# Performance work log

Measured on AMD Instinct MI355X. Metric: run time of the kernel, lower is better.

The kernel has to match this reference:

```python
import jax, jax.numpy as jnp
import numpy as np

B, S, D, H = 4, 4096, 1024, 8
HD = D // H  # head dims, FFT length for circular convolution


def setup_inputs() -> dict:
    key = jax.random.key(0)
    k1, k2, k3 = jax.random.split(key, 3)
    x = jax.random.normal(k1, (B, S, D), dtype=jnp.float32)
    # torch nn.Linear(D, 3D, bias=False) -> store as [D, 3D] for x @ W
    w_qkv = jax.random.normal(k2, (D, 3 * D), dtype=jnp.float32) * (1.0 / np.sqrt(D))
    w_out = jax.random.normal(k3, (D, D), dtype=jnp.float32) * (1.0 / np.sqrt(D))
    return {"x": x, "w_qkv": w_qkv, "w_out": w_out}


def reference(x, w_qkv, w_out):
    # HRR self-attention (causal, norm=False, dropout in eval mode => identity).
    b, s, d = x.shape
    qkv = x @ w_qkv                               # [B,S,3D]
    q, k, v = jnp.split(qkv, 3, axis=-1)
    q = q.reshape(b, s, H, HD)
    k = k.reshape(b, s, H, HD)
    v = v.reshape(b, s, H, HD)
    # Holographic binding: circular convolution k (*) v == ifft(fft(k)*fft(v))
    fq = jnp.fft.fft(q, axis=-1)                  # [B,S,H,HD] complex
    fk = jnp.fft.fft(k, axis=-1)
    fv = jnp.fft.fft(v, axis=-1)
    kv = fk * fv                                  # bound key-value pairs (freq domain)
    kv = jnp.cumsum(kv, axis=1)                   # causal aggregation over sequence
    # Unbinding via circular correlation with the query: ifft(S * conj(fft(q)))
    vals = jnp.fft.ifft(kv * jnp.conj(fq), axis=-1).real.astype(x.dtype)
    vals = vals.reshape(b, s, d)
    return vals @ w_out
```

## Files before the change

### kernel.cpp

```cpp
#include <hip/hip_runtime.h>

static constexpr int BB = 4;
static constexpr int SS = 4096;
static constexpr int DD = 1024;
static constexpr int HH = 8;
static constexpr int HD = 128;
static constexpr int CS = 32;
static constexpr int NCHUNK = SS / CS;
static constexpr int MROWS = BB * SS;

typedef __attribute__((ext_vector_type(8))) short bfrag;
typedef __attribute__((ext_vector_type(4))) float floatx4;

__device__ __forceinline__ float bf2f(unsigned int u) {
    return __uint_as_float((u & 0xFFFFu) << 16);
}
__device__ __forceinline__ unsigned short f2bf(float f) {
    unsigned int x = __float_as_uint(f);
    unsigned int r = x + 0x7FFFu + ((x >> 16) & 1u);
    return (unsigned short)(r >> 16);
}
__device__ __forceinline__ unsigned int pack_rne(float a, float b) {
    return ((unsigned int)f2bf(a)) | (((unsigned int)f2bf(b)) << 16);
}

__device__ __forceinline__ void async_copy16(const void* g, void* l) {
    __builtin_amdgcn_global_load_lds(
        (const __attribute__((address_space(1))) unsigned int*)g,
        (__attribute__((address_space(3))) unsigned int*)l, 16, 0, 0);
}

struct cpx { float re, im; };

__device__ __forceinline__ cpx cadd(cpx a, cpx b) { return {a.re + b.re, a.im + b.im}; }
__device__ __forceinline__ cpx csub(cpx a, cpx b) { return {a.re - b.re, a.im - b.im}; }
__device__ __forceinline__ cpx cmul(cpx a, cpx b) {
    return { fmaf(a.re, b.re, -a.im * b.im), fmaf(a.re, b.im, a.im * b.re) };
}
__device__ __forceinline__ cpx cmul_cj(cpx a, cpx b) {
    return { fmaf(a.re, b.re, a.im * b.im), fmaf(a.im, b.re, -a.re * b.im) };
}
__device__ __forceinline__ cpx shflx(cpx x, int m) {
    return { __shfl_xor(x.re, m), __shfl_xor(x.im, m) };
}
__device__ __forceinline__ cpx shfl_at(cpx x, int src) {
    return { __shfl(x.re, src), __shfl(x.im, src) };
}

__device__ __forceinline__ int pair_lane_even(int l) {
    int m = (int)(__brev((unsigned)l) >> 26);
    int mp = (64 - m) & 63;
    return (int)(__brev((unsigned)mp) >> 26);
}

__device__ __forceinline__ void make_tw(int lane, cpx tw[7]) {
    const float NEG2PI = -6.28318530717958647692f;
    float a0 = NEG2PI * (float)lane * (1.0f / 128.0f);
    tw[0] = { __cosf(a0), __sinf(a0) };
    int d = 32;
#pragma unroll
    for (int s = 1; s <= 6; ++s) {
        int i = lane & (d - 1);
        float a = NEG2PI * (float)i / (float)(2 * d);
        tw[s] = { __cosf(a), __sinf(a) };
        d >>= 1;
    }
}

__device__ __forceinline__ void fft128_fwd(cpx& x0, cpx& x1, const cpx tw[7], int lane) {
    cpx a = x0, b = x1;
    x0 = cadd(a, b);
    x1 = cmul(csub(a, b), tw[0]);
    int d = 32;
#pragma unroll
    for (int s = 1; s <= 6; ++s) {
        const bool up = (lane & d) != 0;
        cpx o0 = shflx(x0, d);
        cpx o1 = shflx(x1, d);
        cpx s0 = cadd(x0, o0);
        cpx s1 = cadd(x1, o1);
        cpx d0 = cmul(csub(o0, x0), tw[s]);
        cpx d1 = cmul(csub(o1, x1), tw[s]);
        x0 = up ? d0 : s0;
        x1 = up ? d1 : s1;
        d >>= 1;
    }
}

__device__ __forceinline__ void fft128_inv(cpx& x0, cpx& x1, const cpx tw[7], int lane) {
    int d = 1;
#pragma unroll
    for (int s = 6; s >= 1; --s) {
        const bool up = (lane & d) != 0;
        cpx o0 = shflx(x0, d);
        cpx o1 = shflx(x1, d);
        cpx b0 = up ? x0 : o0;
        cpx a0 = up ? o0 : x0;
        cpx b1 = up ? x1 : o1;
        cpx a1 = up ? o1 : x1;
        cpx t0 = cmul_cj(b0, tw[s]);
        cpx t1 = cmul_cj(b1, tw[s]);
        x0 = up ? csub(a0, t0) : cadd(a0, t0);
        x1 = up ? csub(a1, t1) : cadd(a1, t1);
        d <<= 1;
    }
    cpx t = cmul_cj(x1, tw[0]);
    cpx a = x0;
    const float inv = 0.0078125f;
    x0 = { (a.re + t.re) * inv, (a.im + t.im) * inv };
    x1 = { (a.re - t.re) * inv, (a.im - t.im) * inv };
}

__global__ __launch_bounds__(256) void convert_bf16(const float* __restrict__ X,
                                                    unsigned short* __restrict__ Y)
{
    const size_t i = ((size_t)blockIdx.x * 256 + threadIdx.x) * 8;
    float4 v0 = *reinterpret_cast<const float4*>(X + i);
    float4 v1 = *reinterpret_cast<const float4*>(X + i + 4);
    uint4 p = { pack_rne(v0.x, v0.y), pack_rne(v0.z, v0.w),
                pack_rne(v1.x, v1.y), pack_rne(v1.z, v1.w) };
    *reinterpret_cast<uint4*>(Y + i) = p;
}

__global__ __launch_bounds__(256) void transpose_rn(const float* __restrict__ W,
                                                    unsigned short* __restrict__ T,
                                                    int K, int N)
{
    __shared__ float tile[32][33];
    const int n0 = blockIdx.x * 32, k0 = blockIdx.y * 32;
    const int r = threadIdx.x >> 5, c = threadIdx.x & 31;
#pragma unroll
    for (int i = 0; i < 4; ++i)
        tile[r + 8 * i][c] = W[(size_t)(k0 + r + 8 * i) * N + n0 + c];
    __syncthreads();
#pragma unroll
    for (int i = 0; i < 4; ++i) {
        float v = tile[c][r + 8 * i];
        T[(size_t)(n0 + r + 8 * i) * K + k0 + c] = f2bf(v);
    }
}

template <typename OutT>
__global__ __launch_bounds__(512, 2) void gemm256(const unsigned short* __restrict__ A,
                                                  const unsigned short* __restrict__ Bt,
                                                  OutT* __restrict__ C,
                                                  int M, int N, int K)
{
    extern __shared__ __align__(16) unsigned short lds[];

    const int tid = threadIdx.x, lane = tid & 63, w = tid >> 6;
    const int wr = w >> 2, wc = w & 3;

    const int nbx = N >> 8;
    const int cpx_ = gridDim.x >> 3;
    const int wg = blockIdx.x;
    const int swz = (wg & 7) * cpx_ + (wg >> 3);
    const int n0 = (swz % nbx) << 8;
    const int m0 = (swz / nbx) << 8;

    const int lr = lane >> 2;
    const int kx = (((lane & 3) ^ ((lane >> 3) & 3)) << 3);
    const unsigned short* gA = A  + (size_t)(m0 + 32 * w + lr) * K + kx;
    const unsigned short* gB = Bt + (size_t)(n0 + 32 * w + lr) * K + kx;

    auto stageA = [&](int buf, int kk, int kelem) {
        unsigned short* dst = lds + buf * 32768 + kk * 8192 + (32 * w) * 32;
        const unsigned short* src = gA + kelem;
        async_copy16(src, dst);
        async_copy16(src + (size_t)16 * K, dst + 512);
    };
    auto stageB = [&](int buf, int kk, int kelem) {
        unsigned short* dst = lds + buf * 32768 + 16384 + kk * 8192 + (32 * w) * 32;
        const unsigned short* src = gB + kelem;
        async_copy16(src, dst);
        async_copy16(src + (size_t)16 * K, dst + 512);
    };

    const int sl = lane >> 4;
    const int xa = ((lane & 15) >> 1) & 3;
    const int soff = ((sl ^ xa) << 3);
    const int ra = (wr * 128 + (lane & 15)) * 32 + soff;
    const int rb = (wc * 64  + (lane & 15)) * 32 + soff;

    floatx4 acc[8][4];
#pragma unroll
    for (int m = 0; m < 8; ++m)
#pragma unroll
        for (int n = 0; n < 4; ++n) { floatx4 z = {0.f, 0.f, 0.f, 0.f}; acc[m][n] = z; }

    const int NT = K >> 6;

    stageA(0, 0, 0);  stageB(0, 0, 0);
    stageA(0, 1, 32); stageB(0, 1, 32);
    if (NT > 1) { stageA(1, 0, 64); stageB(1, 0, 64); }
    asm volatile("s_waitcnt vmcnt(8)" ::: "memory");
    __builtin_amdgcn_s_barrier();

    for (int i = 0; i < NT; ++i) {
        const int bb = (i & 1) * 32768;
        bfrag af0[4], af1[4], bf0[4], bf1[4];

        {
            const unsigned short* pA = lds + bb + ra;
            const unsigned short* pB = lds + bb + 16384 + rb;
#pragma unroll
            for (int m = 0; m < 4; ++m) af0[m] = *reinterpret_cast<const bfrag*>(pA + m * 512);
#pragma unroll
            for (int n = 0; n < 4; ++n) bf0[n] = *reinterpret_cast<const bfrag*>(pB + n * 512);
            if (i + 1 < NT) stageB((i + 1) & 1, 1, (i + 1) * 64 + 32);
            __builtin_amdgcn_s_barrier();
            __builtin_amdgcn_s_setprio(1);
#pragma unroll
            for (int m = 0; m < 4; ++m)
#pragma unroll
                for (int n = 0; n < 4; ++n)
                    acc[m][n] = __builtin_amdgcn_mfma_f32_16x16x32_bf16(af0[m], bf0[n], acc[m][n], 0, 0, 0);
            __builtin_amdgcn_s_setprio(0);
            __builtin_amdgcn_s_barrier();
        }

        {
            const unsigned short* pA = lds + bb + ra + 2048;
#pragma unroll
            for (int m = 0; m < 4; ++m) af1[m] = *reinterpret_cast<const bfrag*>(pA + m * 512);
            if (i + 1 < NT) {
                stageA((i + 1) & 1, 1, (i + 1) * 64 + 32);
                asm volatile("s_waitcnt vmcnt(6)" ::: "memory");
            } else {
                asm volatile("s_waitcnt vmcnt(0)" ::: "memory");
            }
            __builtin_amdgcn_s_barrier();
            __builtin_amdgcn_s_setprio(1);
#pragma unroll
            for (int m = 0; m < 4; ++m)
#pragma unroll
                for (int n = 0; n < 4; ++n)
                    acc[4 + m][n] = __builtin_amdgcn_mfma_f32_16x16x32_bf16(af1[m], bf0[n], acc[4 + m][n], 0, 0, 0);
            __builtin_amdgcn_s_setprio(0);
            __builtin_amdgcn_s_barrier();
        }

        {
            const unsigned short* pA = lds + bb + 8192 + ra;
            const unsigned short* pB = lds + bb + 16384 + 8192 + rb;
#pragma unroll
            for (int m = 0; m < 4; ++m) af0[m] = *reinterpret_cast<const bfrag*>(pA + m * 512);
#pragma unroll
            for (int n = 0; n < 4; ++n) bf1[n] = *reinterpret_cast<const bfrag*>(pB + n * 512);
            if (i + 2 < NT) stageB(i & 1, 0, (i + 2) * 64);
            __builtin_amdgcn_s_barrier();
            __builtin_amdgcn_s_setprio(1);
#pragma unroll
            for (int m = 0; m < 4; ++m)
#pragma unroll
                for (int n = 0; n < 4; ++n)
                    acc[m][n] = __builtin_amdgcn_mfma_f32_16x16x32_bf16(af0[m], bf1[n], acc[m][n], 0, 0, 0);
            __builtin_amdgcn_s_setprio(0);
            __builtin_amdgcn_s_barrier();
        }

        {
            const unsigned short* pA = lds + bb + 8192 + ra + 2048;
#pragma unroll
            for (int m = 0; m < 4; ++m) af1[m] = *reinterpret_cast<const bfrag*>(pA + m * 512);
            if (i + 2 < NT) {
                stageA(i & 1, 0, (i + 2) * 64);
                asm volatile("s_waitcnt vmcnt(6)" ::: "memory");
            } else if (i + 1 < NT) {
                asm volatile("s_waitcnt vmcnt(2)" ::: "memory");
            } else {
                asm volatile("s_waitcnt vmcnt(0)" ::: "memory");
            }
            __builtin_amdgcn_s_barrier();
            __builtin_amdgcn_s_setprio(1);
#pragma unroll
            for (int m = 0; m < 4; ++m)
#pragma unroll
                for (int n = 0; n < 4; ++n)
                    acc[4 + m][n] = __builtin_amdgcn_mfma_f32_16x16x32_bf16(af1[m], bf1[n], acc[4 + m][n], 0, 0, 0);
            __builtin_amdgcn_s_setprio(0);
            __builtin_amdgcn_s_barrier();
        }
    }

    if constexpr (sizeof(OutT) == 2) {
        unsigned short* myt = lds + w * 8192;
#pragma unroll
        for (int m = 0; m < 8; ++m)
#pragma unroll
            for (int n = 0; n < 4; ++n)
#pragma unroll
                for (int r = 0; r < 4; ++r)
                    myt[(m * 16 + sl * 4 + r) * 64 + n * 16 + (lane & 15)] = f2bf(acc[m][n][r]);
        asm volatile("s_waitcnt lgkmcnt(0)" ::: "memory");
#pragma unroll
        for (int c = 0; c < 16; ++c) {
            const int idx = c * 64 + lane;
            const int row = idx >> 3, cc = (idx & 7) << 3;
            uint4 v = *reinterpret_cast<const uint4*>(myt + idx * 8);
            *reinterpret_cast<uint4*>(C + (size_t)(m0 + wr * 128 + row) * N + (n0 + wc * 64 + cc)) = v;
        }
    } else {
        float* myf = reinterpret_cast<float*>(lds) + w * 4096;
#pragma unroll
        for (int pass = 0; pass < 2; ++pass) {
#pragma unroll
            for (int mp = 0; mp < 4; ++mp) {
                const int m = pass * 4 + mp;
#pragma unroll
                for (int n = 0; n < 4; ++n)
#pragma unroll
                    for (int r = 0; r < 4; ++r)
                        myf[(mp * 16 + sl * 4 + r) * 64 + n * 16 + (lane & 15)] = acc[m][n][r];
            }
            asm volatile("s_waitcnt lgkmcnt(0)" ::: "memory");
#pragma unroll
            for (int c = 0; c < 16; ++c) {
                const int idx = c * 64 + lane;
                const int row = idx >> 4;
                const int cc = (idx & 15) << 2;
                float4 v = *reinterpret_cast<const float4*>(myf + row * 64 + cc);
                *reinterpret_cast<float4*>(
                    C + (size_t)(m0 + wr * 128 + pass * 64 + row) * N + (n0 + wc * 64 + cc)) = v;
            }
            asm volatile("s_waitcnt lgkmcnt(0)" ::: "memory");
        }
    }
}

__global__ __launch_bounds__(256) void hrr_phaseA(const unsigned short* __restrict__ qkv,
                                                  unsigned int* __restrict__ P,
                                                  float* __restrict__ totals)
{
    const int blk = blockIdx.x;
    const int bh = blk / NCHUNK;
    const int chunk = blk % NCHUNK;
    const int b = bh >> 3, h = bh & 7;
    const int tid = threadIdx.x;
    const int wave = tid >> 6, lane = tid & 63;

    cpx tw[7];
    make_tw(lane, tw);
    const int pl0 = pair_lane_even(lane);
    const int pl1 = lane ^ 63;

    cpx acc0 = {0.f, 0.f}, acc1 = {0.f, 0.f};
    const int s0 = chunk * CS + wave * (CS / 4);
    for (int i = 0; i < CS / 4; ++i) {
        const int s = s0 + i;
        const unsigned short* base = qkv + (size_t)(b * SS + s) * 3072 + h * 128;
        cpx z0 = { bf2f(base[1024 + lane]),      bf2f(base[2048 + lane]) };
        cpx z1 = { bf2f(base[1024 + 64 + lane]), bf2f(base[2048 + 64 + lane]) };
        fft128_fwd(z0, z1, tw, lane);
        cpx sq0 = cmul(z0, z0);
        cpx sq1 = cmul(z1, z1);
        cpx sp0 = shfl_at(sq0, pl0);
        cpx sp1 = shfl_at(sq1, pl1);
        cpx p0 = { 0.25f * (sq0.im + sp0.im), 0.25f * (sp0.re - sq0.re) };
        cpx p1 = { 0.25f * (sq1.im + sp1.im), 0.25f * (sp1.re - sq1.re) };
        acc0 = cadd(acc0, p0);
        acc1 = cadd(acc1, p1);
        unsigned int* prow = P + ((size_t)bh * SS + s) * 128;
        prow[lane]      = pack_rne(p0.re, p0.im);
        prow[64 + lane] = pack_rne(p1.re, p1.im);
    }

    __shared__ float red[4][256];
    red[wave][lane * 2 + 0] = acc0.re;
    red[wave][lane * 2 + 1] = acc0.im;
    red[wave][128 + lane * 2 + 0] = acc1.re;
    red[wave][128 + lane * 2 + 1] = acc1.im;
    __syncthreads();

    float s4 = red[0][tid] + red[1][tid] + red[2][tid] + red[3][tid];
    totals[((size_t)bh * NCHUNK + chunk) * 256 + tid] = s4;
}

__global__ __launch_bounds__(256) void hrr_phaseB(float* __restrict__ totals)
{
    const int bh = blockIdx.x;
    const int t = threadIdx.x;
    float run = 0.f;
#pragma unroll 4
    for (int c = 0; c < NCHUNK; ++c) {
        const size_t idx = ((size_t)bh * NCHUNK + c) * 256 + t;
        float v = totals[idx];
        totals[idx] = run;
        run += v;
    }
}

__global__ __launch_bounds__(256) void hrr_phaseC(const unsigned short* __restrict__ qkv,
                                                  const unsigned int* __restrict__ P,
                                                  const float* __restrict__ totals,
                                                  unsigned short* __restrict__ vals)
{
    __shared__ float Pf[CS * 256];

    const int blk = blockIdx.x;
    const int bh = blk / NCHUNK;
    const int chunk = blk % NCHUNK;
    const int b = bh >> 3, h = bh & 7;
    const int tid = threadIdx.x;
    const int wave = tid >> 6, lane = tid & 63;

    cpx tw[7];
    make_tw(lane, tw);
    const int pl0 = pair_lane_even(lane);
    const int pl1 = lane ^ 63;

#pragma unroll
    for (int it = 0; it < CS / 4; ++it) {
        const int sl = it * 4 + wave;
        const int s = chunk * CS + sl;
        const unsigned int* prow = P + ((size_t)bh * SS + s) * 128;
        unsigned int a = prow[lane];
        unsigned int c = prow[64 + lane];
        float2 fa = { bf2f(a), bf2f(a >> 16) };
        float2 fc = { bf2f(c), bf2f(c >> 16) };
        *reinterpret_cast<float2*>(&Pf[sl * 256 + 2 * lane]) = fa;
        *reinterpret_cast<float2*>(&Pf[sl * 256 + 128 + 2 * lane]) = fc;
    }
    __syncthreads();

    {
        float run = totals[((size_t)bh * NCHUNK + chunk) * 256 + tid];
#pragma unroll 8
        for (int s = 0; s < CS; ++s) {
            run += Pf[s * 256 + tid];
            Pf[s * 256 + tid] = run;
        }
    }
    __syncthreads();

    for (int i = 0; i < CS / 8; ++i) {
        const int sl = wave * (CS / 4) + 2 * i;
        const int s1 = chunk * CS + sl;
        const unsigned short* b1 = qkv + (size_t)(b * SS + s1) * 3072 + h * 128;
        const unsigned short* b2 = b1 + 3072;
        cpx z0 = { bf2f(b1[lane]),      bf2f(b2[lane]) };
        cpx z1 = { bf2f(b1[64 + lane]), bf2f(b2[64 + lane]) };
        fft128_fwd(z0, z1, tw, lane);
        cpx B0 = shfl_at(z0, pl0);
        cpx B1 = shfl_at(z1, pl1);
        cpx cf1_0 = { 0.5f * (z0.re + B0.re), 0.5f * (B0.im - z0.im) };
        cpx cf1_1 = { 0.5f * (z1.re + B1.re), 0.5f * (B1.im - z1.im) };
        cpx cf2_0 = { 0.5f * (z0.im + B0.im), 0.5f * (z0.re - B0.re) };
        cpx cf2_1 = { 0.5f * (z1.im + B1.im), 0.5f * (z1.re - B1.re) };

        const float* r1 = &Pf[sl * 256];
        const float* r2 = r1 + 256;
        float2 t0 = *reinterpret_cast<const float2*>(&r1[2 * lane]);
        float2 t1 = *reinterpret_cast<const float2*>(&r1[128 + 2 * lane]);
        float2 t2 = *reinterpret_cast<const float2*>(&r2[2 * lane]);
        float2 t3 = *reinterpret_cast<const float2*>(&r2[128 + 2 * lane]);
        cpx C1_0 = { t0.x, t0.y }, C1_1 = { t1.x, t1.y };
        cpx C2_0 = { t2.x, t2.y }, C2_1 = { t3.x, t3.y };

        cpx a0 = cmul(C1_0, cf1_0), w0 = cmul(C2_0, cf2_0);
        cpx a1 = cmul(C1_1, cf1_1), w1 = cmul(C2_1, cf2_1);
        cpx u0 = { a0.re - w0.im, a0.im + w0.re };
        cpx u1 = { a1.re - w1.im, a1.im + w1.re };
        fft128_inv(u0, u1, tw, lane);

        unsigned short* o1 = vals + (size_t)(b * SS + s1) * DD + h * 128;
        unsigned short* o2 = o1 + DD;
        o1[lane]      = f2bf(u0.re);
        o1[64 + lane] = f2bf(u1.re);
        o2[lane]      = f2bf(u0.im);
        o2[64 + lane] = f2bf(u1.im);
    }
}

extern "C" void kernel_launch(void* const* d_in, const int* in_sizes, int n_in,
                              void* d_out, int out_size, void* d_ws, size_t ws_size,
                              hipStream_t stream) {
    const float* x     = (const float*)d_in[0];
    const float* w_qkv = (const float*)d_in[1];
    const float* w_out = (const float*)d_in[2];
    float* out = (float*)d_out;

    unsigned short* qkv  = (unsigned short*)d_ws;
    unsigned short* xb   = qkv + (size_t)MROWS * 3072;
    unsigned short* vals = xb + (size_t)MROWS * DD;
    unsigned int* P      = (unsigned int*)(vals + (size_t)MROWS * DD);
    float* totals        = (float*)(P + (size_t)32 * SS * 128);
    unsigned short* wqkvt = (unsigned short*)(totals + (size_t)32 * NCHUNK * 256);
    unsigned short* woutt = wqkvt + (size_t)3072 * 1024;

    static bool attr_done = false;
    if (!attr_done) {
        hipFuncSetAttribute(reinterpret_cast<const void*>(gemm256<unsigned short>),
                            hipFuncAttributeMaxDynamicSharedMemorySize, 131072);
        hipFuncSetAttribute(reinterpret_cast<const void*>(gemm256<float>),
                            hipFuncAttributeMaxDynamicSharedMemorySize, 131072);
        attr_done = true;
    }

    convert_bf16<<<(MROWS * DD) / (256 * 8), 256, 0, stream>>>(x, xb);
    transpose_rn<<<dim3(3072 / 32, 1024 / 32), 256, 0, stream>>>(w_qkv, wqkvt, 1024, 3072);
    transpose_rn<<<dim3(1024 / 32, 1024 / 32), 256, 0, stream>>>(w_out, woutt, 1024, 1024);

    gemm256<unsigned short><<<(3072 / 256) * (MROWS / 256), 512, 131072, stream>>>(
        xb, wqkvt, qkv, MROWS, 3072, DD);

    hrr_phaseA<<<BB * HH * NCHUNK, 256, 0, stream>>>(qkv, P, totals);

    hrr_phaseB<<<BB * HH, 256, 0, stream>>>(totals);

    hrr_phaseC<<<BB * HH * NCHUNK, 256, 0, stream>>>(qkv, P, totals, vals);

    gemm256<float><<<(DD / 256) * (MROWS / 256), 512, 131072, stream>>>(
        vals, woutt, out, MROWS, DD, DD);
}
```

Measured before the change: 369.0 us.

## Stage HRR scan inputs and outputs through LDS with async 16-byte copies

```diff
diff --git a/kernel.cpp b/kernel.cpp
--- a/kernel.cpp
+++ b/kernel.cpp
@@ -332,6 +332,9 @@
                                                   unsigned int* __restrict__ P,
                                                   float* __restrict__ totals)
 {
+    __shared__ __align__(16) unsigned short Sk[CS * 128];
+    __shared__ __align__(16) unsigned short Sv[CS * 128];
+
     const int blk = blockIdx.x;
     const int bh = blk / NCHUNK;
     const int chunk = blk % NCHUNK;
@@ -339,18 +342,33 @@
     const int tid = threadIdx.x;
     const int wave = tid >> 6, lane = tid & 63;
 
+    {
+        const size_t rowbase = (size_t)(b * SS + chunk * CS) * 3072 + h * 128;
+#pragma unroll
+        for (int q = 0; q < 2; ++q) {
+            const int r = 8 * wave + 4 * q + (lane >> 4);
+            const unsigned short* srcK = qkv + rowbase + (size_t)r * 3072 + 1024 + (lane & 15) * 8;
+            const unsigned short* srcV = srcK + 1024;
+            async_copy16(srcK, Sk + (8 * wave + 4 * q) * 128);
+            async_copy16(srcV, Sv + (8 * wave + 4 * q) * 128);
+        }
+    }
+
     cpx tw[7];
     make_tw(lane, tw);
     const int pl0 = pair_lane_even(lane);
     const int pl1 = lane ^ 63;
 
+    __syncthreads();
+
     cpx acc0 = {0.f, 0.f}, acc1 = {0.f, 0.f};
     const int s0 = chunk * CS + wave * (CS / 4);
     for (int i = 0; i < CS / 4; ++i) {
-        const int s = s0 + i;
-        const unsigned short* base = qkv + (size_t)(b * SS + s) * 3072 + h * 128;
-        cpx z0 = { bf2f(base[1024 + lane]),      bf2f(base[2048 + lane]) };
-        cpx z1 = { bf2f(base[1024 + 64 + lane]), bf2f(base[2048 + 64 + lane]) };
+        const int sl = wave * (CS / 4) + i;
+        const unsigned short* kk = Sk + sl * 128;
+        const unsigned short* vv = Sv + sl * 128;
+        cpx z0 = { bf2f(kk[lane]),      bf2f(vv[lane]) };
+        cpx z1 = { bf2f(kk[64 + lane]), bf2f(vv[64 + lane]) };
         fft128_fwd(z0, z1, tw, lane);
         cpx sq0 = cmul(z0, z0);
         cpx sq1 = cmul(z1, z1);
@@ -360,7 +378,7 @@
         cpx p1 = { 0.25f * (sq1.im + sp1.im), 0.25f * (sp1.re - sq1.re) };
         acc0 = cadd(acc0, p0);
         acc1 = cadd(acc1, p1);
-        unsigned int* prow = P + ((size_t)bh * SS + s) * 128;
+        unsigned int* prow = P + ((size_t)bh * SS + s0 + i) * 128;
         prow[lane]      = pack_rne(p0.re, p0.im);
         prow[64 + lane] = pack_rne(p1.re, p1.im);
     }
@@ -376,10 +394,10 @@
     totals[((size_t)bh * NCHUNK + chunk) * 256 + tid] = s4;
 }
 
-__global__ __launch_bounds__(256) void hrr_phaseB(float* __restrict__ totals)
+__global__ __launch_bounds__(64) void hrr_phaseB(float* __restrict__ totals)
 {
-    const int bh = blockIdx.x;
-    const int t = threadIdx.x;
+    const int bh = blockIdx.x >> 2;
+    const int t = (blockIdx.x & 3) * 64 + threadIdx.x;
     float run = 0.f;
 #pragma unroll 4
     for (int c = 0; c < NCHUNK; ++c) {
@@ -396,6 +414,8 @@
                                                   unsigned short* __restrict__ vals)
 {
     __shared__ float Pf[CS * 256];
+    __shared__ __align__(16) unsigned short Sq[CS * 128];
+    __shared__ __align__(16) unsigned short So[CS * 128];
 
     const int blk = blockIdx.x;
     const int bh = blk / NCHUNK;
@@ -404,6 +424,16 @@
     const int tid = threadIdx.x;
     const int wave = tid >> 6, lane = tid & 63;
 
+    {
+        const size_t rowbase = (size_t)(b * SS + chunk * CS) * 3072 + h * 128;
+#pragma unroll
+        for (int q = 0; q < 2; ++q) {
+            const int r = 8 * wave + 4 * q + (lane >> 4);
+            const unsigned short* srcQ = qkv + rowbase + (size_t)r * 3072 + (lane & 15) * 8;
+            async_copy16(srcQ, Sq + (8 * wave + 4 * q) * 128);
+        }
+    }
+
     cpx tw[7];
     make_tw(lane, tw);
     const int pl0 = pair_lane_even(lane);
@@ -414,12 +444,9 @@
         const int sl = it * 4 + wave;
         const int s = chunk * CS + sl;
         const unsigned int* prow = P + ((size_t)bh * SS + s) * 128;
-        unsigned int a = prow[lane];
-        unsigned int c = prow[64 + lane];
-        float2 fa = { bf2f(a), bf2f(a >> 16) };
-        float2 fc = { bf2f(c), bf2f(c >> 16) };
-        *reinterpret_cast<float2*>(&Pf[sl * 256 + 2 * lane]) = fa;
-        *reinterpret_cast<float2*>(&Pf[sl * 256 + 128 + 2 * lane]) = fc;
+        uint2 pp = *reinterpret_cast<const uint2*>(prow + 2 * lane);
+        float4 f = { bf2f(pp.x), bf2f(pp.x >> 16), bf2f(pp.y), bf2f(pp.y >> 16) };
+        *reinterpret_cast<float4*>(&Pf[sl * 256 + 4 * lane]) = f;
     }
     __syncthreads();
 
@@ -435,11 +462,10 @@
 
     for (int i = 0; i < CS / 8; ++i) {
         const int sl = wave * (CS / 4) + 2 * i;
-        const int s1 = chunk * CS + sl;
-        const unsigned short* b1 = qkv + (size_t)(b * SS + s1) * 3072 + h * 128;
-        const unsigned short* b2 = b1 + 3072;
-        cpx z0 = { bf2f(b1[lane]),      bf2f(b2[lane]) };
-        cpx z1 = { bf2f(b1[64 + lane]), bf2f(b2[64 + lane]) };
+        const unsigned short* q1 = Sq + sl * 128;
+        const unsigned short* q2 = q1 + 128;
+        cpx z0 = { bf2f(q1[lane]),      bf2f(q2[lane]) };
+        cpx z1 = { bf2f(q1[64 + lane]), bf2f(q2[64 + lane]) };
         fft128_fwd(z0, z1, tw, lane);
         cpx B0 = shfl_at(z0, pl0);
         cpx B1 = shfl_at(z1, pl1);
@@ -463,12 +489,23 @@
         cpx u1 = { a1.re - w1.im, a1.im + w1.re };
         fft128_inv(u0, u1, tw, lane);
 
-        unsigned short* o1 = vals + (size_t)(b * SS + s1) * DD + h * 128;
-        unsigned short* o2 = o1 + DD;
+        unsigned short* o1 = So + sl * 128;
+        unsigned short* o2 = o1 + 128;
         o1[lane]      = f2bf(u0.re);
         o1[64 + lane] = f2bf(u1.re);
         o2[lane]      = f2bf(u0.im);
         o2[64 + lane] = f2bf(u1.im);
+    }
+    __syncthreads();
+
+#pragma unroll
+    for (int rr = 0; rr < 2; ++rr) {
+        const int idx = rr * 256 + tid;
+        const int row = idx >> 4;
+        const int c8 = (idx & 15) << 3;
+        uint4 v = *reinterpret_cast<const uint4*>(So + row * 128 + c8);
+        *reinterpret_cast<uint4*>(
+            vals + (size_t)(b * SS + chunk * CS + row) * DD + h * 128 + c8) = v;
     }
 }
 
@@ -506,7 +543,7 @@
 
     hrr_phaseA<<<BB * HH * NCHUNK, 256, 0, stream>>>(qkv, P, totals);
 
-    hrr_phaseB<<<BB * HH, 256, 0, stream>>>(totals);
+    hrr_phaseB<<<BB * HH * 4, 64, 0, stream>>>(totals);
 
     hrr_phaseC<<<BB * HH * NCHUNK, 256, 0, stream>>>(qkv, P, totals, vals);
 
```

After: 390.6 us. +5.8%, slower.
